# Optimization experiments

Hardware: AMD Instinct MI355X
Metric: run time of the kernel (lower is better)

The kernel has to match this reference:

```python
import jax, jax.numpy as jnp
import numpy as np

N_HEAD = 16
D_MODEL = 1024
D_HEAD = 64
SEQ = 2048
BATCH = 4
EPS = 1e-5


def setup_inputs() -> dict:
    key = jax.random.key(0)
    k1, k2, k3, k4 = jax.random.split(key, 4)
    s = 1.0 / np.sqrt(D_MODEL)
    return {
        "h": jax.random.normal(k1, (SEQ, BATCH, D_MODEL), jnp.float32),
        "Wq": jax.random.normal(k2, (D_MODEL, N_HEAD * D_HEAD), jnp.float32) * s,
        "Wkv": jax.random.normal(k3, (D_MODEL, 2 * N_HEAD * D_HEAD), jnp.float32) * s,
        "Wo": jax.random.normal(k4, (N_HEAD * D_HEAD, D_MODEL), jnp.float32) * s,
        "gamma": jnp.ones((D_MODEL,), jnp.float32),
        "beta": jnp.zeros((D_MODEL,), jnp.float32),
    }


def _layer_norm(x, gamma, beta):
    mu = jnp.mean(x, axis=-1, keepdims=True)
    var = jnp.mean(jnp.square(x - mu), axis=-1, keepdims=True)
    return (x - mu) * jax.lax.rsqrt(var + EPS) * gamma + beta


def reference(h, Wq, Wkv, Wo, gamma, beta):
    # h: [i, b, d_model]; no mems, post-lnorm, dropout=0 (eval)
    scale = 1.0 / np.sqrt(D_HEAD)
    q = (h @ Wq).reshape(SEQ, BATCH, N_HEAD, D_HEAD)
    kv = h @ Wkv
    k, v = jnp.split(kv, 2, axis=-1)
    k = k.reshape(SEQ, BATCH, N_HEAD, D_HEAD)
    v = v.reshape(SEQ, BATCH, N_HEAD, D_HEAD)
    # attention scores [i, j, b, n]
    score = jnp.einsum('ibnd,jbnd->ijbn', q, k) * scale
    prob = jax.nn.softmax(score, axis=1)
    attn_vec = jnp.einsum('ijbn,jbnd->ibnd', prob, v)
    attn_vec = attn_vec.reshape(SEQ, BATCH, N_HEAD * D_HEAD)
    attn_out = attn_vec @ Wo
    return _layer_norm(h + attn_out, gamma, beta)
```

## Files before the change

### kernel.cpp

```cpp
#include <hip/hip_runtime.h>
#include <hip/hip_bf16.h>


typedef __attribute__((ext_vector_type(4))) float f32x4;
typedef __attribute__((ext_vector_type(16))) float f32x16;
typedef __attribute__((ext_vector_type(8))) short s16x8;
typedef unsigned short u16;
typedef unsigned int u32;
typedef __attribute__((ext_vector_type(4))) u16 u16x4;
typedef __attribute__((ext_vector_type(2))) u32 u32x2;

#define SEQ   2048
#define BATCH 4
#define NH    16
#define DH    64
#define DM    1024
#define ROWS  (SEQ*BATCH)

#define QSCALE 0.18033688011112042f
#define DEFER_THR 11.5416f

__device__ inline u16 f2bf(float x) {
    u32 u = __float_as_uint(x);
    u += 0x7FFF + ((u >> 16) & 1);
    return (u16)(u >> 16);
}

__device__ inline u32 cvtpk_bf16(float lo, float hi_) {
    u32 r;
    asm("v_cvt_pk_bf16_f32 %0, %1, %2" : "=v"(r) : "v"(lo), "v"(hi_));
    return r;
}

__device__ inline void gload16(const void* g, void* l) {
    __builtin_amdgcn_global_load_lds((const __attribute__((address_space(1))) void*)g,
                                     (__attribute__((address_space(3))) void*)l, 16, 0, 0);
}

__global__ __launch_bounds__(256) void conv_f32_bf16(const float* __restrict__ src,
                                                     u16* __restrict__ dst, int n4) {
    int idx = blockIdx.x * 256 + threadIdx.x;
    if (idx >= n4) return;
    f32x4 v = ((const f32x4*)src)[idx];
    u16x4 o;
    #pragma unroll
    for (int j = 0; j < 4; ++j) o[j] = f2bf(v[j]);
    ((u16x4*)dst)[idx] = o;
}

__global__ __launch_bounds__(1024) void transconv_k(const float* __restrict__ src,
                                                    u16* __restrict__ dst, int K, int N) {
    __shared__ float t[32][33];
    int tx = threadIdx.x, ty = threadIdx.y;
    int nt = blockIdx.x * 32, kt = blockIdx.y * 32;
    t[ty][tx] = src[(size_t)(kt + ty) * N + nt + tx];
    __syncthreads();
    dst[(size_t)(nt + ty) * K + kt + tx] = f2bf(t[tx][ty]);
}

template<int MODE>
__global__ __launch_bounds__(256) void gemm_k(const u16* __restrict__ A,
                                              const u16* __restrict__ BT,
                                              const float* __restrict__ hres,
                                              u16* __restrict__ o_q,
                                              u16* __restrict__ o_k,
                                              u16* __restrict__ o_v,
                                              float* __restrict__ o_f) {
    __shared__ u16 Al[2][128 * 32];
    __shared__ u16 Bl[2][128 * 32];
    int lane = threadIdx.x & 63, wid = threadIdx.x >> 6;
    int lr = lane & 15, lg = lane >> 4;
    int m0 = blockIdx.x * 128, n0 = blockIdx.y * 128;
    int wr = wid >> 1, wc = wid & 1;

    f32x4 acc[4][4];
    #pragma unroll
    for (int mi = 0; mi < 4; ++mi)
        #pragma unroll
        for (int ni = 0; ni < 4; ++ni)
            #pragma unroll
            for (int rr = 0; rr < 4; ++rr) acc[mi][ni][rr] = 0.f;

#define GEMM_STAGE(bb, kt) do {                                                    \
    int kk = (kt) * 32;                                                            \
    _Pragma("unroll")                                                              \
    for (int it = 0; it < 2; ++it) {                                               \
        int c = (int)threadIdx.x + it * 256;                                       \
        int row = c >> 2, sub = c & 3;                                             \
        int sc = (sub ^ (row & 3)) * 8;                                            \
        gload16(A  + (size_t)(m0 + row) * 1024 + kk + sc,                          \
                &Al[bb][(wid * 64 + it * 256) * 8]);                               \
        gload16(BT + (size_t)(n0 + row) * 1024 + kk + sc,                          \
                &Bl[bb][(wid * 64 + it * 256) * 8]);                               \
    } } while (0)

    GEMM_STAGE(0, 0);
    __syncthreads();
    int cur = 0;
    for (int kt = 0; kt < 32; ++kt) {
        if (kt + 1 < 32) GEMM_STAGE(cur ^ 1, kt + 1);
        const u16* Ab = &Al[cur][0];
        const u16* Bb = &Bl[cur][0];
        s16x8 af[4], bf[4];
        #pragma unroll
        for (int mi = 0; mi < 4; ++mi) {
            int row = wr * 64 + mi * 16 + lr;
            af[mi] = *(const s16x8*)(Ab + row * 32 + ((lg ^ (row & 3)) * 8));
        }
        #pragma unroll
        for (int ni = 0; ni < 4; ++ni) {
            int row = wc * 64 + ni * 16 + lr;
            bf[ni] = *(const s16x8*)(Bb + row * 32 + ((lg ^ (row & 3)) * 8));
        }
        #pragma unroll
        for (int mi = 0; mi < 4; ++mi)
            #pragma unroll
            for (int ni = 0; ni < 4; ++ni)
                acc[mi][ni] = __builtin_amdgcn_mfma_f32_16x16x32_bf16(af[mi], bf[ni], acc[mi][ni], 0, 0, 0);
        __syncthreads();
        cur ^= 1;
    }
#undef GEMM_STAGE

    #pragma unroll
    for (int mi = 0; mi < 4; ++mi)
        #pragma unroll
        for (int rr = 0; rr < 4; ++rr) {
            int row = m0 + wr * 64 + mi * 16 + lg * 4 + rr;
            int ib = row >> 2, bb = row & 3;
            #pragma unroll
            for (int ni = 0; ni < 4; ++ni) {
                int col = n0 + wc * 64 + ni * 16 + lr;
                float v = acc[mi][ni][rr];
                if (MODE == 0) {
                    if (col < 1024) {
                        int nn = col >> 6, dd = col & 63;
                        o_q[(((size_t)(bb * 16 + nn) * SEQ + ib) << 6) + dd] = f2bf(v * QSCALE);
                    } else if (col < 2048) {
                        int c2 = col - 1024, nn = c2 >> 6, dd = c2 & 63;
                        o_k[(((size_t)(bb * 16 + nn) * SEQ + ib) << 6) + dd] = f2bf(v);
                    } else {
                        int c2 = col - 2048, nn = c2 >> 6, dd = c2 & 63;
                        o_v[(((size_t)(bb * 16 + nn) * SEQ + ib) << 6) + dd] = f2bf(v);
                    }
                } else {
                    size_t off = (size_t)row * 1024 + col;
                    o_f[off] = v + hres[off];
                }
            }
        }
}

__global__ __launch_bounds__(256) void vtrans_k(const u16* __restrict__ vn, u16* __restrict__ vT) {
    __shared__ u16 t[64][65];
    int p = blockIdx.y, j0 = blockIdx.x * 64;
    const u16* src = vn + ((size_t)p * SEQ + j0) * 64;
    #pragma unroll
    for (int it = 0; it < 2; ++it) {
        int idx = threadIdx.x + it * 256;
        int row = idx >> 3, ch = idx & 7;
        s16x8 v = *(const s16x8*)(src + (size_t)row * 64 + ch * 8);
        #pragma unroll
        for (int jj = 0; jj < 8; ++jj) t[row][ch * 8 + jj] = (u16)v[jj];
    }
    __syncthreads();
    u16* dst = vT + (size_t)p * 64 * SEQ + j0;
    #pragma unroll
    for (int it = 0; it < 2; ++it) {
        int idx = threadIdx.x + it * 256;
        int d = idx >> 3, ch = idx & 7;
        s16x8 o;
        #pragma unroll
        for (int jj = 0; jj < 8; ++jj) o[jj] = (short)t[ch * 8 + jj][d];
        *(s16x8*)(dst + (size_t)d * SEQ + ch * 8) = o;
    }
}

__global__ __launch_bounds__(256) void attn_k(const u16* __restrict__ qw, const u16* __restrict__ kw,
                                              const u16* __restrict__ vT, u16* __restrict__ avw) {
    __shared__ u16 Kl[2][64 * 64];
    __shared__ u16 Vl[2][64 * 64];
    int lane = threadIdx.x & 63, wid = threadIdx.x >> 6;
    int l31 = lane & 31, hi = lane >> 5;
    int f = blockIdx.x;
    int pair = (f & 7) * 8 + ((f >> 3) & 7);
    int qt = f >> 6;
    int b = pair >> 4, n = pair & 15;
    int q0 = qt * 128 + wid * 32;

    const u16* Q  = qw + ((size_t)pair * SEQ + q0) * 64;
    const u16* Kg = kw + (size_t)pair * SEQ * 64;
    const u16* Vg = vT + (size_t)pair * 64 * SEQ;

    s16x8 qf[4];
    #pragma unroll
    for (int kt = 0; kt < 4; ++kt)
        qf[kt] = *(const s16x8*)(Q + (size_t)l31 * 64 + kt * 16 + hi * 8);

    f32x16 Ot[2];
    #pragma unroll
    for (int dt = 0; dt < 2; ++dt)
        #pragma unroll
        for (int r = 0; r < 16; ++r) Ot[dt][r] = 0.f;
    float m = -3.0e38f, lsum = 0.f;

#define ATTN_STAGE(bb, j0s) do {                                                   \
    _Pragma("unroll")                                                              \
    for (int it = 0; it < 2; ++it) {                                               \
        int c = (int)threadIdx.x + it * 256;                                       \
        int row = c >> 3, cl = c & 7;                                              \
        int sc = (cl ^ (row & 7)) * 8;                                             \
        gload16(Kg + (size_t)((j0s) + row) * 64 + sc,                              \
                &Kl[bb][(wid * 64 + it * 256) * 8]);                               \
        gload16(Vg + (size_t)row * SEQ + (j0s) + sc,                               \
                &Vl[bb][(wid * 64 + it * 256) * 8]);                               \
    } } while (0)

    ATTN_STAGE(0, 0);
    __syncthreads();
    int cur = 0;

    for (int jt = 0; jt < 32; ++jt) {
        int j0 = jt * 64;
        if (jt + 1 < 32) ATTN_STAGE(cur ^ 1, j0 + 64);
        const u16* Kb = &Kl[cur][0];
        const u16* Vb = &Vl[cur][0];

        f32x16 s0, s1;
        #pragma unroll
        for (int r = 0; r < 16; ++r) { s0[r] = 0.f; s1[r] = 0.f; }
        #pragma unroll
        for (int kt = 0; kt < 4; ++kt) {
            int cg = kt * 2 + hi;
            int r0 = l31;
            s16x8 ka = *(const s16x8*)(Kb + r0 * 64 + ((cg ^ (r0 & 7)) * 8));
            s0 = __builtin_amdgcn_mfma_f32_32x32x16_bf16(ka, qf[kt], s0, 0, 0, 0);
        }
        #pragma unroll
        for (int kt = 0; kt < 4; ++kt) {
            int cg = kt * 2 + hi;
            int r1 = 32 + l31;
            s16x8 ka = *(const s16x8*)(Kb + r1 * 64 + ((cg ^ (r1 & 7)) * 8));
            s1 = __builtin_amdgcn_mfma_f32_32x32x16_bf16(ka, qf[kt], s1, 0, 0, 0);
        }

        float mx[16];
        #pragma unroll
        for (int r = 0; r < 16; ++r) mx[r] = fmaxf(s0[r], s1[r]);
        #pragma unroll
        for (int st = 8; st >= 1; st >>= 1)
            #pragma unroll
            for (int r = 0; r < st; ++r) mx[r] = fmaxf(mx[r], mx[r + st]);
        float pmax = mx[0];

        if (!__all(pmax - m <= DEFER_THR)) {
            float pmo = fmaxf(pmax, __shfl_xor(pmax, 32, 64));
            float mn = fmaxf(m, pmo);
            float sf = __builtin_amdgcn_exp2f(m - mn);
            m = mn;
            lsum *= sf;
            #pragma unroll
            for (int dt = 0; dt < 2; ++dt)
                #pragma unroll
                for (int r = 0; r < 16; ++r) Ot[dt][r] *= sf;
        }

        u32 pk[16];
        float ps[4] = {0.f, 0.f, 0.f, 0.f};
        #pragma unroll
        for (int mp = 0; mp < 8; ++mp) {
            float a0 = __builtin_amdgcn_exp2f(s0[2 * mp] - m);
            float a1 = __builtin_amdgcn_exp2f(s0[2 * mp + 1] - m);
            ps[mp & 3] += a0 + a1;
            pk[mp] = cvtpk_bf16(a0, a1);
            float b0 = __builtin_amdgcn_exp2f(s1[2 * mp] - m);
            float b1 = __builtin_amdgcn_exp2f(s1[2 * mp + 1] - m);
            ps[(mp & 3) ^ 2] += b0 + b1;
            pk[8 + mp] = cvtpk_bf16(b0, b1);
        }
        lsum += (ps[0] + ps[1]) + (ps[2] + ps[3]);

        #pragma unroll
        for (int t = 0; t < 2; ++t)
            #pragma unroll
            for (int kt2 = 0; kt2 < 2; ++kt2) {
                int base = t * 8 + kt2 * 4;
                u32x2 w02 = __builtin_amdgcn_permlane32_swap(pk[base + 0], pk[base + 2], false, false);
                u32x2 w13 = __builtin_amdgcn_permlane32_swap(pk[base + 1], pk[base + 3], false, false);
                union { u32 w[4]; s16x8 v; } fr;
                fr.w[0] = w02[0]; fr.w[1] = w13[0]; fr.w[2] = w02[1]; fr.w[3] = w13[1];
                #pragma unroll
                for (int dt = 0; dt < 2; ++dt) {
                    int rv = dt * 32 + l31;
                    int cgv = t * 4 + kt2 * 2 + hi;
                    s16x8 va = *(const s16x8*)(Vb + rv * 64 + ((cgv ^ (rv & 7)) * 8));
                    Ot[dt] = __builtin_amdgcn_mfma_f32_32x32x16_bf16(va, fr.v, Ot[dt], 0, 0, 0);
                }
            }
        __syncthreads();
        cur ^= 1;
    }
#undef ATTN_STAGE

    float L = lsum + __shfl_xor(lsum, 32, 64);
    float inv = 1.f / L;
    int i = q0 + l31;
    size_t rowo = (size_t)(i * 4 + b) * 1024 + n * 64;
    #pragma unroll
    for (int dt = 0; dt < 2; ++dt)
        #pragma unroll
        for (int rq = 0; rq < 4; ++rq) {
            int dbase = dt * 32 + rq * 8 + hi * 4;
            u16x4 o;
            #pragma unroll
            for (int e = 0; e < 4; ++e) o[e] = f2bf(Ot[dt][rq * 4 + e] * inv);
            *(u16x4*)(avw + rowo + dbase) = o;
        }
}

__global__ __launch_bounds__(256) void ln_k(float* __restrict__ y,
                                            const float* __restrict__ g,
                                            const float* __restrict__ be) {
    int row = blockIdx.x, t = threadIdx.x;
    f32x4 v = ((const f32x4*)(y + (size_t)row * 1024))[t];
    float s = v[0] + v[1] + v[2] + v[3];
    float q = v[0] * v[0] + v[1] * v[1] + v[2] * v[2] + v[3] * v[3];
    #pragma unroll
    for (int msk = 1; msk < 64; msk <<= 1) {
        s += __shfl_xor(s, msk, 64);
        q += __shfl_xor(q, msk, 64);
    }
    __shared__ float ss[4], qq[4];
    int w = t >> 6;
    if ((t & 63) == 0) { ss[w] = s; qq[w] = q; }
    __syncthreads();
    s = ss[0] + ss[1] + ss[2] + ss[3];
    q = qq[0] + qq[1] + qq[2] + qq[3];
    float mean = s * (1.f / 1024.f);
    float var = q * (1.f / 1024.f) - mean * mean;
    float rstd = rsqrtf(var + 1e-5f);
    f32x4 gv = ((const f32x4*)g)[t];
    f32x4 bv = ((const f32x4*)be)[t];
    f32x4 o;
    #pragma unroll
    for (int j = 0; j < 4; ++j) o[j] = (v[j] - mean) * rstd * gv[j] + bv[j];
    ((f32x4*)(y + (size_t)row * 1024))[t] = o;
}

extern "C" void kernel_launch(void* const* d_in, const int* in_sizes, int n_in,
                              void* d_out, int out_size, void* d_ws, size_t ws_size,
                              hipStream_t stream) {
    const float* h     = (const float*)d_in[0];
    const float* Wq    = (const float*)d_in[1];
    const float* Wkv   = (const float*)d_in[2];
    const float* Wo    = (const float*)d_in[3];
    const float* gamma = (const float*)d_in[4];
    const float* beta  = (const float*)d_in[5];
    float* out = (float*)d_out;

    char* w = (char*)d_ws;
    u16* hb   = (u16*)w; w += (size_t)ROWS * DM * 2;
    u16* WqT  = (u16*)w; w += (size_t)DM * DM * 2;
    u16* WkvT = (u16*)w; w += (size_t)2 * DM * DM * 2;
    u16* WoT  = (u16*)w; w += (size_t)DM * DM * 2;
    u16* qw   = (u16*)w; w += (size_t)64 * SEQ * 64 * 2;
    u16* kw   = (u16*)w; w += (size_t)64 * SEQ * 64 * 2;
    u16* vn   = (u16*)w; w += (size_t)64 * SEQ * 64 * 2;
    u16* vT   = (u16*)w; w += (size_t)64 * SEQ * 64 * 2;
    u16* avw  = vn;

    conv_f32_bf16<<<ROWS * DM / 4 / 256, 256, 0, stream>>>(h, hb, ROWS * DM / 4);
    dim3 b32(32, 32);
    transconv_k<<<dim3(32, 32), b32, 0, stream>>>(Wq, WqT, 1024, 1024);
    transconv_k<<<dim3(64, 32), b32, 0, stream>>>(Wkv, WkvT, 1024, 2048);
    transconv_k<<<dim3(32, 32), b32, 0, stream>>>(Wo, WoT, 1024, 1024);

    gemm_k<0><<<dim3(64, 24), 256, 0, stream>>>(hb, WqT, nullptr, qw, kw, vn, nullptr);
    vtrans_k<<<dim3(32, 64), 256, 0, stream>>>(vn, vT);
    attn_k<<<1024, 256, 0, stream>>>(qw, kw, vT, avw);
    gemm_k<2><<<dim3(64, 8), 256, 0, stream>>>(avw, WoT, h, nullptr, nullptr, nullptr, out);
    ln_k<<<ROWS, 256, 0, stream>>>(out, gamma, beta);
}
```

Before: 363.1 us.

## Fuse V transpose into QKV GEMM epilogue and vectorize output stores

Swaps the MFMA operand order so each lane holds four consecutive output columns. The epilogue can then write packed 4-element bf16 stores for Q and K, and float4 read-add-write for the residual GEMM. V is written directly in transposed layout from the GEMM epilogue, which removes the separate vtrans kernel, its launch, and one round trip of V through memory. The transposed V stores are scalar and strided by SEQ, which may coalesce poorly.

```diff
diff --git a/kernel.cpp b/kernel.cpp
--- a/kernel.cpp
+++ b/kernel.cpp
@@ -116,63 +116,45 @@
         for (int mi = 0; mi < 4; ++mi)
             #pragma unroll
             for (int ni = 0; ni < 4; ++ni)
-                acc[mi][ni] = __builtin_amdgcn_mfma_f32_16x16x32_bf16(af[mi], bf[ni], acc[mi][ni], 0, 0, 0);
+                acc[mi][ni] = __builtin_amdgcn_mfma_f32_16x16x32_bf16(bf[ni], af[mi], acc[mi][ni], 0, 0, 0);
         __syncthreads();
         cur ^= 1;
     }
 #undef GEMM_STAGE
 
     #pragma unroll
-    for (int mi = 0; mi < 4; ++mi)
-        #pragma unroll
-        for (int rr = 0; rr < 4; ++rr) {
-            int row = m0 + wr * 64 + mi * 16 + lg * 4 + rr;
-            int ib = row >> 2, bb = row & 3;
-            #pragma unroll
-            for (int ni = 0; ni < 4; ++ni) {
-                int col = n0 + wc * 64 + ni * 16 + lr;
-                float v = acc[mi][ni][rr];
-                if (MODE == 0) {
-                    if (col < 1024) {
-                        int nn = col >> 6, dd = col & 63;
-                        o_q[(((size_t)(bb * 16 + nn) * SEQ + ib) << 6) + dd] = f2bf(v * QSCALE);
-                    } else if (col < 2048) {
-                        int c2 = col - 1024, nn = c2 >> 6, dd = c2 & 63;
-                        o_k[(((size_t)(bb * 16 + nn) * SEQ + ib) << 6) + dd] = f2bf(v);
-                    } else {
-                        int c2 = col - 2048, nn = c2 >> 6, dd = c2 & 63;
-                        o_v[(((size_t)(bb * 16 + nn) * SEQ + ib) << 6) + dd] = f2bf(v);
-                    }
+    for (int mi = 0; mi < 4; ++mi) {
+        int row = m0 + wr * 64 + mi * 16 + lr;
+        int ib = row >> 2, bb = row & 3;
+        #pragma unroll
+        for (int ni = 0; ni < 4; ++ni) {
+            int ncol = n0 + wc * 64 + ni * 16 + lg * 4;
+            f32x4 v = acc[mi][ni];
+            if (MODE == 0) {
+                if (ncol < 1024) {
+                    int nn = ncol >> 6, dd = ncol & 63;
+                    u16x4 o;
+                    #pragma unroll
+                    for (int e = 0; e < 4; ++e) o[e] = f2bf(v[e] * QSCALE);
+                    *(u16x4*)(o_q + (((size_t)(bb * 16 + nn) * SEQ + ib) << 6) + dd) = o;
+                } else if (ncol < 2048) {
+                    int c2 = ncol - 1024, nn = c2 >> 6, dd = c2 & 63;
+                    u16x4 o;
+                    #pragma unroll
+                    for (int e = 0; e < 4; ++e) o[e] = f2bf(v[e]);
+                    *(u16x4*)(o_k + (((size_t)(bb * 16 + nn) * SEQ + ib) << 6) + dd) = o;
                 } else {
-                    size_t off = (size_t)row * 1024 + col;
-                    o_f[off] = v + hres[off];
+                    int c2 = ncol - 2048, nn = c2 >> 6, dd = c2 & 63;
+                    size_t base = ((size_t)(bb * 16 + nn) * 64 + dd) * SEQ + ib;
+                    #pragma unroll
+                    for (int e = 0; e < 4; ++e) o_v[base + (size_t)e * SEQ] = f2bf(v[e]);
                 }
+            } else {
+                size_t off = (size_t)row * 1024 + ncol;
+                f32x4 hv = *(const f32x4*)(hres + off);
+                *(f32x4*)(o_f + off) = v + hv;
             }
         }
-}
-
-__global__ __launch_bounds__(256) void vtrans_k(const u16* __restrict__ vn, u16* __restrict__ vT) {
-    __shared__ u16 t[64][65];
-    int p = blockIdx.y, j0 = blockIdx.x * 64;
-    const u16* src = vn + ((size_t)p * SEQ + j0) * 64;
-    #pragma unroll
-    for (int it = 0; it < 2; ++it) {
-        int idx = threadIdx.x + it * 256;
-        int row = idx >> 3, ch = idx & 7;
-        s16x8 v = *(const s16x8*)(src + (size_t)row * 64 + ch * 8);
-        #pragma unroll
-        for (int jj = 0; jj < 8; ++jj) t[row][ch * 8 + jj] = (u16)v[jj];
-    }
-    __syncthreads();
-    u16* dst = vT + (size_t)p * 64 * SEQ + j0;
-    #pragma unroll
-    for (int it = 0; it < 2; ++it) {
-        int idx = threadIdx.x + it * 256;
-        int d = idx >> 3, ch = idx & 7;
-        s16x8 o;
-        #pragma unroll
-        for (int jj = 0; jj < 8; ++jj) o[jj] = (short)t[ch * 8 + jj][d];
-        *(s16x8*)(dst + (size_t)d * SEQ + ch * 8) = o;
     }
 }
 
@@ -365,9 +347,8 @@
     u16* WoT  = (u16*)w; w += (size_t)DM * DM * 2;
     u16* qw   = (u16*)w; w += (size_t)64 * SEQ * 64 * 2;
     u16* kw   = (u16*)w; w += (size_t)64 * SEQ * 64 * 2;
-    u16* vn   = (u16*)w; w += (size_t)64 * SEQ * 64 * 2;
+    u16* avw  = (u16*)w; w += (size_t)64 * SEQ * 64 * 2;
     u16* vT   = (u16*)w; w += (size_t)64 * SEQ * 64 * 2;
-    u16* avw  = vn;
 
     conv_f32_bf16<<<ROWS * DM / 4 / 256, 256, 0, stream>>>(h, hb, ROWS * DM / 4);
     dim3 b32(32, 32);
@@ -375,8 +356,7 @@
     transconv_k<<<dim3(64, 32), b32, 0, stream>>>(Wkv, WkvT, 1024, 2048);
     transconv_k<<<dim3(32, 32), b32, 0, stream>>>(Wo, WoT, 1024, 1024);
 
-    gemm_k<0><<<dim3(64, 24), 256, 0, stream>>>(hb, WqT, nullptr, qw, kw, vn, nullptr);
-    vtrans_k<<<dim3(32, 64), 256, 0, stream>>>(vn, vT);
+    gemm_k<0><<<dim3(64, 24), 256, 0, stream>>>(hb, WqT, nullptr, qw, kw, vT, nullptr);
     attn_k<<<1024, 256, 0, stream>>>(qw, kw, vT, avw);
     gemm_k<2><<<dim3(64, 8), 256, 0, stream>>>(avw, WoT, h, nullptr, nullptr, nullptr, out);
     ln_k<<<ROWS, 256, 0, stream>>>(out, gamma, beta);
```

After: 335.6 us. 1.08x faster.
